# Performance work log

Hardware: AMD Instinct MI355X
Metric: run time of the kernel (lower is better)

The kernel has to match this reference:

```python
import jax, jax.numpy as jnp
import numpy as np

NUM_SEGMENTS = 1024  # batch_size (number of graphs), fixed at trace time


def setup_inputs() -> dict:
    key = jax.random.key(0)
    k_x, k_b, k_w1, k_b1, k_w2, k_b2 = jax.random.split(key, 6)
    num_nodes, hidden_dim = 500000, 256
    x = jax.random.normal(k_x, (num_nodes, hidden_dim), dtype=jnp.float32)
    batch = jnp.sort(jax.random.randint(k_b, (num_nodes,), 0, NUM_SEGMENTS, dtype=jnp.int32))
    # attention MLP params: Linear(hidden, hidden//2) -> Tanh -> Linear(hidden//2, 1)
    h2 = hidden_dim // 2
    s1 = 1.0 / np.sqrt(hidden_dim)
    s2 = 1.0 / np.sqrt(h2)
    W1 = jax.random.uniform(k_w1, (hidden_dim, h2), jnp.float32, -s1, s1)
    b1 = jax.random.uniform(k_b1, (h2,), jnp.float32, -s1, s1)
    W2 = jax.random.uniform(k_w2, (h2, 1), jnp.float32, -s2, s2)
    b2 = jax.random.uniform(k_b2, (1,), jnp.float32, -s2, s2)
    return {"x": x, "batch": batch, "W1": W1, "b1": b1, "W2": W2, "b2": b2}


def reference(x, batch, W1, b1, W2, b2):
    # attention scores: small MLP -> (num_nodes, 1)
    scores = jnp.tanh(x @ W1 + b1) @ W2 + b2  # (N, 1)
    s = scores[:, 0]  # (N,)
    # segment-wise stable softmax
    seg_max = jax.ops.segment_max(s, batch, num_segments=NUM_SEGMENTS)  # (B,)
    exp_s = jnp.exp(s - seg_max[batch])  # (N,)
    seg_sum = jax.ops.segment_sum(exp_s, batch, num_segments=NUM_SEGMENTS)  # (B,)
    attn = exp_s / (seg_sum[batch] + 1e-8)  # (N,)
    # weighted scatter-add pooling -> (B, hidden_dim)
    weighted_x = x * attn[:, None]
    out = jax.ops.segment_sum(weighted_x, batch, num_segments=NUM_SEGMENTS)
    return out
```

## Files before the change

kernel.cpp:

```cpp
#include <hip/hip_runtime.h>
#include <hip/hip_bf16.h>
#include <math.h>

#define NSEG 1024
#define HID  256
#define H2   128
#define TM   32
#define LROW 260

typedef __attribute__((ext_vector_type(8))) __bf16 bf16x8;
typedef __attribute__((ext_vector_type(4))) float  f32x4;

__device__ __forceinline__ bf16x8 pack8(f32x4 lo, f32x4 hi) {
    bf16x8 b;
    b[0] = (__bf16)lo[0]; b[1] = (__bf16)lo[1]; b[2] = (__bf16)lo[2]; b[3] = (__bf16)lo[3];
    b[4] = (__bf16)hi[0]; b[5] = (__bf16)hi[1]; b[6] = (__bf16)hi[2]; b[7] = (__bf16)hi[3];
    return b;
}

__global__ __launch_bounds__(256, 2)
void attn_pool_kernel(const float* __restrict__ x, const int* __restrict__ batch,
                      const float* __restrict__ W1, const float* __restrict__ b1,
                      const float* __restrict__ W2, float* __restrict__ out, int N)
{
    __shared__ __align__(16) float xs[2][TM * LROW];
    __shared__ float s_part[4][TM];
    __shared__ float s_fin[TM];

    const int tid  = threadIdx.x;
    const int wid  = tid >> 6;
    const int lane = tid & 63;
    const int l15  = lane & 15;
    const int lg   = lane >> 4;
    const int seg  = blockIdx.x;

    int lo = 0, hi = N;
    while (lo < hi) { int mid = (lo + hi) >> 1; if (batch[mid] < seg) lo = mid + 1; else hi = mid; }
    const int start = lo;
    hi = N;
    while (lo < hi) { int mid = (lo + hi) >> 1; if (batch[mid] <= seg) lo = mid + 1; else hi = mid; }
    const int end = lo;

    bf16x8 bfrag[8][2];
    #pragma unroll
    for (int kt = 0; kt < 8; ++kt) {
        #pragma unroll
        for (int nt = 0; nt < 2; ++nt) {
            const int col = wid * 32 + nt * 16 + l15;
            const int kb  = kt * 32 + lg * 8;
            bf16x8 b;
            #pragma unroll
            for (int j = 0; j < 8; ++j) b[j] = (__bf16)W1[(kb + j) * H2 + col];
            bfrag[kt][nt] = b;
        }
    }
    float b1v[2], w2v[2];
    #pragma unroll
    for (int nt = 0; nt < 2; ++nt) {
        const int col = wid * 32 + nt * 16 + l15;
        b1v[nt] = b1[col];
        w2v[nt] = W2[col];
    }

    float m_run = -INFINITY, l_run = 0.f, acc_d = 0.f;

    const int cnt    = end - start;
    const int ntiles = (cnt + TM - 1) / TM;

    f32x4 st[8];

    if (ntiles > 0) {
        #pragma unroll
        for (int q = 0; q < 8; ++q) {
            int idx = q * 256 + tid;
            int r = idx >> 6, c4 = idx & 63;
            int gr = start + r; if (gr > end - 1) gr = end - 1;
            st[q] = *(const f32x4*)&x[gr * HID + c4 * 4];
        }
        #pragma unroll
        for (int q = 0; q < 8; ++q) {
            int idx = q * 256 + tid;
            int r = idx >> 6, c4 = idx & 63;
            *(f32x4*)&xs[0][r * LROW + c4 * 4] = st[q];
        }
    }
    __syncthreads();

    for (int t = 0; t < ntiles; ++t) {
        const int  cur      = t & 1;
        const int  row0     = start + t * TM;
        const bool has_next = (t + 1) < ntiles;
        const float* xb     = xs[cur];

        if (has_next) {
            const int nrow0 = row0 + TM;
            #pragma unroll
            for (int q = 0; q < 8; ++q) {
                int idx = q * 256 + tid;
                int r = idx >> 6, c4 = idx & 63;
                int gr = nrow0 + r; if (gr > end - 1) gr = end - 1;
                st[q] = *(const f32x4*)&x[gr * HID + c4 * 4];
            }
        }

        f32x4 acc[2][2] = {};
        #pragma unroll
        for (int kt = 0; kt < 8; ++kt) {
            bf16x8 a[2];
            #pragma unroll
            for (int mt = 0; mt < 2; ++mt) {
                const float* p = &xb[(mt * 16 + l15) * LROW + kt * 32 + lg * 8];
                f32x4 lo4 = *(const f32x4*)p;
                f32x4 hi4 = *(const f32x4*)(p + 4);
                a[mt] = pack8(lo4, hi4);
            }
            #pragma unroll
            for (int mt = 0; mt < 2; ++mt)
                #pragma unroll
                for (int nt = 0; nt < 2; ++nt)
                    acc[mt][nt] = __builtin_amdgcn_mfma_f32_16x16x32_bf16(
                        a[mt], bfrag[kt][nt], acc[mt][nt], 0, 0, 0);
        }

        #pragma unroll
        for (int mt = 0; mt < 2; ++mt) {
            #pragma unroll
            for (int r = 0; r < 4; ++r) {
                float p = 0.f;
                #pragma unroll
                for (int nt = 0; nt < 2; ++nt) {
                    float h  = acc[mt][nt][r] + b1v[nt];
                    float e2 = __expf(fminf(2.f * h, 80.f));
                    float th = __fdividef(e2 - 1.f, e2 + 1.f);
                    p = fmaf(th, w2v[nt], p);
                }
                p += __shfl_xor(p, 1);
                p += __shfl_xor(p, 2);
                p += __shfl_xor(p, 4);
                p += __shfl_xor(p, 8);
                if (l15 == 0) s_part[wid][mt * 16 + lg * 4 + r] = p;
            }
        }
        __syncthreads();
        if (tid < TM) {
            float s = s_part[0][tid] + s_part[1][tid] + s_part[2][tid] + s_part[3][tid];
            if (row0 + tid >= end) s = -1e30f;
            s_fin[tid] = s;
        }
        __syncthreads();

        float tmax = -1e30f;
        #pragma unroll
        for (int i = 0; i < TM; ++i) tmax = fmaxf(tmax, s_fin[i]);
        const float m_new = fmaxf(m_run, tmax);
        const float scale = __expf(m_run - m_new);
        acc_d *= scale;
        l_run *= scale;
        #pragma unroll
        for (int i = 0; i < TM; ++i) {
            float e = __expf(s_fin[i] - m_new);
            l_run += e;
            acc_d  = fmaf(e, xb[i * LROW + tid], acc_d);
        }
        m_run = m_new;

        if (has_next) {
            #pragma unroll
            for (int q = 0; q < 8; ++q) {
                int idx = q * 256 + tid;
                int r = idx >> 6, c4 = idx & 63;
                *(f32x4*)&xs[cur ^ 1][r * LROW + c4 * 4] = st[q];
            }
        }
        __syncthreads();
    }

    out[seg * HID + tid] = acc_d / (l_run + 1e-8f);
}

extern "C" void kernel_launch(void* const* d_in, const int* in_sizes, int n_in,
                              void* d_out, int out_size, void* d_ws, size_t ws_size,
                              hipStream_t stream) {
    const float* x     = (const float*)d_in[0];
    const int*   batch = (const int*)d_in[1];
    const float* W1    = (const float*)d_in[2];
    const float* b1    = (const float*)d_in[3];
    const float* W2    = (const float*)d_in[4];
    float* out = (float*)d_out;
    const int N = in_sizes[1];

    attn_pool_kernel<<<NSEG, 256, 0, stream>>>(x, batch, W1, b1, W2, out, N);
}
```

Baseline: 714.3 us.

## Stage x tiles as bf16 in swizzled LDS and double block width to 512

Converts each x tile to bf16 once at LDS store time, using an XOR swizzled layout without padding. This halves LDS footprint and removes the per-MFMA fp32-to-bf16 packing. Blocks grow to 512 threads: each wave owns 16 of the 128 hidden columns, and the weighted pooling splits tile rows across two thread halves that are combined at the end. The pooled sum now reads bf16-rounded x instead of fp32, which lowers accuracy of the output.

```diff
diff --git a/kernel.cpp b/kernel.cpp
--- a/kernel.cpp
+++ b/kernel.cpp
@@ -2,14 +2,16 @@
 #include <hip/hip_bf16.h>
 #include <math.h>
 
-#define NSEG 1024
-#define HID  256
-#define H2   128
-#define TM   32
-#define LROW 260
+#define NSEG  1024
+#define HID   256
+#define H2    128
+#define TM    32
+#define BLOCK 512
 
 typedef __attribute__((ext_vector_type(8))) __bf16 bf16x8;
 typedef __attribute__((ext_vector_type(4))) float  f32x4;
+typedef unsigned int   uint32;
+typedef unsigned short ushort16;
 
 __device__ __forceinline__ bf16x8 pack8(f32x4 lo, f32x4 hi) {
     bf16x8 b;
@@ -18,122 +20,110 @@
     return b;
 }
 
-__global__ __launch_bounds__(256, 2)
+__global__ __launch_bounds__(BLOCK, 4)
 void attn_pool_kernel(const float* __restrict__ x, const int* __restrict__ batch,
                       const float* __restrict__ W1, const float* __restrict__ b1,
                       const float* __restrict__ W2, float* __restrict__ out, int N)
 {
-    __shared__ __align__(16) float xs[2][TM * LROW];
-    __shared__ float s_part[4][TM];
-    __shared__ float s_fin[TM];
+    __shared__ __align__(16) unsigned short xs[2][TM * HID];
+    __shared__ float s_part[8][TM];
+    __shared__ __align__(16) float s_fin[TM];
+    __shared__ float acc_hi[HID];
+    __shared__ float l_hi;
 
     const int tid  = threadIdx.x;
     const int wid  = tid >> 6;
     const int lane = tid & 63;
     const int l15  = lane & 15;
     const int lg   = lane >> 4;
+    const int s7   = l15 & 7;
     const int seg  = blockIdx.x;
 
     int lo = 0, hi = N;
-    while (lo < hi) { int mid = (lo + hi) >> 1; if (batch[mid] < seg) lo = mid + 1; else hi = mid; }
+    while (lo < hi) { int mid = (lo + hi) >> 1; if (batch[mid] <  seg) lo = mid + 1; else hi = mid; }
     const int start = lo;
     hi = N;
     while (lo < hi) { int mid = (lo + hi) >> 1; if (batch[mid] <= seg) lo = mid + 1; else hi = mid; }
     const int end = lo;
 
-    bf16x8 bfrag[8][2];
+    const int col = wid * 16 + l15;
+    bf16x8 bfrag[8];
     #pragma unroll
     for (int kt = 0; kt < 8; ++kt) {
-        #pragma unroll
-        for (int nt = 0; nt < 2; ++nt) {
-            const int col = wid * 32 + nt * 16 + l15;
-            const int kb  = kt * 32 + lg * 8;
-            bf16x8 b;
-            #pragma unroll
-            for (int j = 0; j < 8; ++j) b[j] = (__bf16)W1[(kb + j) * H2 + col];
-            bfrag[kt][nt] = b;
-        }
-    }
-    float b1v[2], w2v[2];
-    #pragma unroll
-    for (int nt = 0; nt < 2; ++nt) {
-        const int col = wid * 32 + nt * 16 + l15;
-        b1v[nt] = b1[col];
-        w2v[nt] = W2[col];
-    }
-
-    float m_run = -INFINITY, l_run = 0.f, acc_d = 0.f;
+        bf16x8 b;
+        #pragma unroll
+        for (int j = 0; j < 8; ++j) b[j] = (__bf16)W1[(kt * 32 + lg * 8 + j) * H2 + col];
+        bfrag[kt] = b;
+    }
+    const float b1v = b1[col];
+    const float w2v = W2[col];
 
     const int cnt    = end - start;
     const int ntiles = (cnt + TM - 1) / TM;
 
-    f32x4 st[8];
+    const int sr  = tid >> 5;
+    const int suc = tid & 31;
+    const int so0 = ((sr * 32) + (suc ^ (sr & 7))) * 16;
+    const int so1 = so0 + 16 * 32 * 16;
+
+    char* const xs0 = (char*)&xs[0][0];
+    f32x4 ld0, ld1, ld2, ld3;
 
     if (ntiles > 0) {
-        #pragma unroll
-        for (int q = 0; q < 8; ++q) {
-            int idx = q * 256 + tid;
-            int r = idx >> 6, c4 = idx & 63;
-            int gr = start + r; if (gr > end - 1) gr = end - 1;
-            st[q] = *(const f32x4*)&x[gr * HID + c4 * 4];
-        }
-        #pragma unroll
-        for (int q = 0; q < 8; ++q) {
-            int idx = q * 256 + tid;
-            int r = idx >> 6, c4 = idx & 63;
-            *(f32x4*)&xs[0][r * LROW + c4 * 4] = st[q];
-        }
+        const int last = end - 1;
+        int gr0 = start + sr;      if (gr0 > last) gr0 = last;
+        int gr1 = start + sr + 16; if (gr1 > last) gr1 = last;
+        const float* p0 = x + (size_t)gr0 * HID + suc * 8;
+        const float* p1 = x + (size_t)gr1 * HID + suc * 8;
+        ld0 = *(const f32x4*)p0; ld1 = *(const f32x4*)(p0 + 4);
+        ld2 = *(const f32x4*)p1; ld3 = *(const f32x4*)(p1 + 4);
+        *(bf16x8*)(xs0 + so0) = pack8(ld0, ld1);
+        *(bf16x8*)(xs0 + so1) = pack8(ld2, ld3);
     }
     __syncthreads();
+
+    float m_run = -INFINITY, l_run = 0.f, acc_d = 0.f;
+    const int d     = tid & (HID - 1);
+    const int du    = d >> 3;
+    const int dl    = d & 7;
+    const int row_h = (tid >> 8) * 16;
 
     for (int t = 0; t < ntiles; ++t) {
         const int  cur      = t & 1;
         const int  row0     = start + t * TM;
         const bool has_next = (t + 1) < ntiles;
-        const float* xb     = xs[cur];
+        const char* xb = xs0 + cur * (TM * HID * 2);
+        const unsigned short* xbu = (const unsigned short*)xb;
 
         if (has_next) {
-            const int nrow0 = row0 + TM;
-            #pragma unroll
-            for (int q = 0; q < 8; ++q) {
-                int idx = q * 256 + tid;
-                int r = idx >> 6, c4 = idx & 63;
-                int gr = nrow0 + r; if (gr > end - 1) gr = end - 1;
-                st[q] = *(const f32x4*)&x[gr * HID + c4 * 4];
-            }
-        }
-
-        f32x4 acc[2][2] = {};
+            const int last = end - 1;
+            int gr0 = row0 + TM + sr;      if (gr0 > last) gr0 = last;
+            int gr1 = row0 + TM + sr + 16; if (gr1 > last) gr1 = last;
+            const float* p0 = x + (size_t)gr0 * HID + suc * 8;
+            const float* p1 = x + (size_t)gr1 * HID + suc * 8;
+            ld0 = *(const f32x4*)p0; ld1 = *(const f32x4*)(p0 + 4);
+            ld2 = *(const f32x4*)p1; ld3 = *(const f32x4*)(p1 + 4);
+        }
+
+        f32x4 acc0 = {0.f, 0.f, 0.f, 0.f}, acc1 = {0.f, 0.f, 0.f, 0.f};
+        const char* arow = xb + l15 * 512;
         #pragma unroll
         for (int kt = 0; kt < 8; ++kt) {
-            bf16x8 a[2];
-            #pragma unroll
-            for (int mt = 0; mt < 2; ++mt) {
-                const float* p = &xb[(mt * 16 + l15) * LROW + kt * 32 + lg * 8];
-                f32x4 lo4 = *(const f32x4*)p;
-                f32x4 hi4 = *(const f32x4*)(p + 4);
-                a[mt] = pack8(lo4, hi4);
-            }
-            #pragma unroll
-            for (int mt = 0; mt < 2; ++mt)
-                #pragma unroll
-                for (int nt = 0; nt < 2; ++nt)
-                    acc[mt][nt] = __builtin_amdgcn_mfma_f32_16x16x32_bf16(
-                        a[mt], bfrag[kt][nt], acc[mt][nt], 0, 0, 0);
+            const int sw = (((kt * 4) + lg) ^ s7) * 16;
+            bf16x8 a0 = *(const bf16x8*)(arow + sw);
+            bf16x8 a1 = *(const bf16x8*)(arow + 8192 + sw);
+            acc0 = __builtin_amdgcn_mfma_f32_16x16x32_bf16(a0, bfrag[kt], acc0, 0, 0, 0);
+            acc1 = __builtin_amdgcn_mfma_f32_16x16x32_bf16(a1, bfrag[kt], acc1, 0, 0, 0);
         }
 
         #pragma unroll
         for (int mt = 0; mt < 2; ++mt) {
             #pragma unroll
             for (int r = 0; r < 4; ++r) {
-                float p = 0.f;
-                #pragma unroll
-                for (int nt = 0; nt < 2; ++nt) {
-                    float h  = acc[mt][nt][r] + b1v[nt];
-                    float e2 = __expf(fminf(2.f * h, 80.f));
-                    float th = __fdividef(e2 - 1.f, e2 + 1.f);
-                    p = fmaf(th, w2v[nt], p);
-                }
+                float h  = (mt ? acc1[r] : acc0[r]) + b1v;
+                float e2 = __expf(fminf(2.f * h, 80.f));
+                float th = __fdividef(e2 - 1.f, e2 + 1.f);
+                float p  = th * w2v;
                 p += __shfl_xor(p, 1);
                 p += __shfl_xor(p, 2);
                 p += __shfl_xor(p, 4);
@@ -143,7 +133,9 @@
         }
         __syncthreads();
         if (tid < TM) {
-            float s = s_part[0][tid] + s_part[1][tid] + s_part[2][tid] + s_part[3][tid];
+            float s = s_part[0][tid];
+            #pragma unroll
+            for (int w = 1; w < 8; ++w) s += s_part[w][tid];
             if (row0 + tid >= end) s = -1e30f;
             s_fin[tid] = s;
         }
@@ -151,31 +143,52 @@
 
         float tmax = -1e30f;
         #pragma unroll
-        for (int i = 0; i < TM; ++i) tmax = fmaxf(tmax, s_fin[i]);
+        for (int i = 0; i < 8; ++i) {
+            f32x4 v = *(const f32x4*)&s_fin[i * 4];
+            tmax = fmaxf(tmax, fmaxf(fmaxf(v[0], v[1]), fmaxf(v[2], v[3])));
+        }
         const float m_new = fmaxf(m_run, tmax);
         const float scale = __expf(m_run - m_new);
         acc_d *= scale;
         l_run *= scale;
-        #pragma unroll
-        for (int i = 0; i < TM; ++i) {
-            float e = __expf(s_fin[i] - m_new);
-            l_run += e;
-            acc_d  = fmaf(e, xb[i * LROW + tid], acc_d);
+
+        f32x4 sh0 = *(const f32x4*)&s_fin[row_h + 0];
+        f32x4 sh1 = *(const f32x4*)&s_fin[row_h + 4];
+        f32x4 sh2 = *(const f32x4*)&s_fin[row_h + 8];
+        f32x4 sh3 = *(const f32x4*)&s_fin[row_h + 12];
+        #pragma unroll
+        for (int q = 0; q < 4; ++q) {
+            f32x4 sv = (q == 0) ? sh0 : (q == 1) ? sh1 : (q == 2) ? sh2 : sh3;
+            #pragma unroll
+            for (int j = 0; j < 4; ++j) {
+                const int rr  = q * 4 + j;
+                const float e = __expf(sv[j] - m_new);
+                l_run += e;
+                const int idx = (row_h + rr) * HID + ((du ^ (rr & 7)) << 3) + dl;
+                const float xv = __uint_as_float(((uint32)xbu[idx]) << 16);
+                acc_d = fmaf(e, xv, acc_d);
+            }
         }
         m_run = m_new;
 
         if (has_next) {
-            #pragma unroll
-            for (int q = 0; q < 8; ++q) {
-                int idx = q * 256 + tid;
-                int r = idx >> 6, c4 = idx & 63;
-                *(f32x4*)&xs[cur ^ 1][r * LROW + c4 * 4] = st[q];
-            }
+            char* xn = xs0 + (cur ^ 1) * (TM * HID * 2);
+            *(bf16x8*)(xn + so0) = pack8(ld0, ld1);
+            *(bf16x8*)(xn + so1) = pack8(ld2, ld3);
         }
         __syncthreads();
     }
 
-    out[seg * HID + tid] = acc_d / (l_run + 1e-8f);
+    if (tid >= HID) {
+        acc_hi[d] = acc_d;
+        if (tid == HID) l_hi = l_run;
+    }
+    __syncthreads();
+    if (tid < HID) {
+        const float a = acc_d + acc_hi[tid];
+        const float l = l_run + l_hi;
+        out[seg * HID + tid] = a / (l + 1e-8f);
+    }
 }
 
 extern "C" void kernel_launch(void* const* d_in, const int* in_sizes, int n_in,
@@ -189,5 +202,5 @@
     float* out = (float*)d_out;
     const int N = in_sizes[1];
 
-    attn_pool_kernel<<<NSEG, 256, 0, stream>>>(x, batch, W1, b1, W2, out, N);
+    attn_pool_kernel<<<NSEG, BLOCK, 0, stream>>>(x, batch, W1, b1, W2, out, N);
 }
```

After: 921.4 us. 1.29x slower.
